# Performance work log

Hardware: AMD Instinct MI355X
Metric: run time of the kernel (lower is better)

The kernel has to match this reference:

```python
import jax, jax.numpy as jnp
import numpy as np

DT = 0.01  # ODE integration step (init kwarg dt)
B, S, I, H, O = 64, 4096, 128, 256, 128


def setup_inputs() -> dict:
    key = jax.random.key(0)
    k0, k1, k2, k3 = jax.random.split(key, 4)
    x = jax.random.normal(k0, (B, S, I), jnp.float32)
    # LTC cell parameters: Linear(in+hidden -> hidden), per-neuron tau and A
    W = jax.random.normal(k1, (I + H, H), jnp.float32) / np.sqrt(I + H)
    b = jnp.zeros((H,), jnp.float32)
    tau = jnp.ones((H,), jnp.float32)
    A = jax.random.normal(k2, (H,), jnp.float32)
    # output Linear(hidden -> out)
    Wo = jax.random.normal(k3, (H, O), jnp.float32) / np.sqrt(H)
    bo = jnp.zeros((O,), jnp.float32)
    return {"x": x, "W": W, "b": b, "tau": tau, "A": A, "Wo": Wo, "bo": bo}


def reference(x, W, b, tau, A, Wo, bo):
    # x: [B, S, I]; recurrence over S with LTC fused semi-implicit ODE step.
    h0 = jnp.zeros((x.shape[0], W.shape[1]), x.dtype)

    def step(h, x_t):
        # f = tanh(Linear([x_t, h]))
        f = jnp.tanh(jnp.concatenate([x_t, h], axis=-1) @ W + b)  # [B, H]
        # fused LTC solver: h' = (h + dt*f*A) / (1 + dt*(1/tau + f))
        h_new = (h + DT * f * A) / (1.0 + DT * (1.0 / tau + f))
        return h_new, None

    h_final, _ = jax.lax.scan(step, h0, jnp.swapaxes(x, 0, 1))  # scan over time
    return h_final @ Wo + bo  # [B, O]
```

## Files before the change

### kernel.cpp

```cpp
#include <hip/hip_runtime.h>
#include <math.h>

#define DT    0.01f
#define B_    64
#define S_    4096
#define I_    128
#define H_    256
#define O_    128

typedef _Float16 f16x8 __attribute__((ext_vector_type(8)));
typedef float    f32x4 __attribute__((ext_vector_type(4)));

#define RPB 64

__global__ __launch_bounds__(256, 2) void xproj_kernel(
    const float* __restrict__ x, const float* __restrict__ W,
    const float* __restrict__ bias, float* __restrict__ xp)
{
  __shared__ __align__(16) float xs[RPB][I_];
  const int j = threadIdx.x;

  float w[I_];
#pragma unroll
  for (int k = 0; k < I_; ++k) w[k] = W[k * H_ + j];
  const float bj = bias[j];

  const size_t row0 = (size_t)blockIdx.x * RPB;

  const float4* src4 = (const float4*)(x + row0 * I_);
  float4* xs4 = (float4*)&xs[0][0];
#pragma unroll
  for (int i = 0; i < (RPB * I_ / 4) / 256; ++i)
    xs4[j + i * 256] = src4[j + i * 256];
  __syncthreads();

  for (int r = 0; r < RPB; r += 4) {
    float a0 = bj, a1 = bj, a2 = bj, a3 = bj;
    const float4* r0 = (const float4*)xs[r + 0];
    const float4* r1 = (const float4*)xs[r + 1];
    const float4* r2 = (const float4*)xs[r + 2];
    const float4* r3 = (const float4*)xs[r + 3];
#pragma unroll
    for (int k4 = 0; k4 < I_ / 4; ++k4) {
      float4 v0 = r0[k4], v1 = r1[k4], v2 = r2[k4], v3 = r3[k4];
      a0 = fmaf(v0.x, w[4*k4+0], a0); a0 = fmaf(v0.y, w[4*k4+1], a0);
      a0 = fmaf(v0.z, w[4*k4+2], a0); a0 = fmaf(v0.w, w[4*k4+3], a0);
      a1 = fmaf(v1.x, w[4*k4+0], a1); a1 = fmaf(v1.y, w[4*k4+1], a1);
      a1 = fmaf(v1.z, w[4*k4+2], a1); a1 = fmaf(v1.w, w[4*k4+3], a1);
      a2 = fmaf(v2.x, w[4*k4+0], a2); a2 = fmaf(v2.y, w[4*k4+1], a2);
      a2 = fmaf(v2.z, w[4*k4+2], a2); a2 = fmaf(v2.w, w[4*k4+3], a2);
      a3 = fmaf(v3.x, w[4*k4+0], a3); a3 = fmaf(v3.y, w[4*k4+1], a3);
      a3 = fmaf(v3.z, w[4*k4+2], a3); a3 = fmaf(v3.w, w[4*k4+3], a3);
    }
    xp[(row0 + r + 0) * H_ + j] = a0;
    xp[(row0 + r + 1) * H_ + j] = a1;
    xp[(row0 + r + 2) * H_ + j] = a2;
    xp[(row0 + r + 3) * H_ + j] = a3;
  }
}

__global__ __launch_bounds__(1024, 4) void ltc_main(
    const float* __restrict__ xp, const float* __restrict__ W,
    const float* __restrict__ tau, const float* __restrict__ A,
    const float* __restrict__ Wo, const float* __restrict__ bo,
    float* __restrict__ out)
{
  const int b  = blockIdx.x;
  const int t  = threadIdx.x;
  const int wv = t >> 6;
  const int l  = t & 63;
  const int g  = l >> 4;
  const int c  = l & 15;
  const int o  = wv * 16 + c;

  f16x8 bw[8];
#pragma unroll
  for (int kt = 0; kt < 8; ++kt)
#pragma unroll
    for (int j = 0; j < 8; ++j)
      bw[kt][j] = (_Float16)W[(I_ + kt * 32 + g * 8 + j) * H_ + o];

  __shared__ __align__(16) _Float16 hs[2][H_];
  __shared__ float hfin[H_];

  const float dtA  = DT * A[o];
  const float base = 1.0f + DT * (1.0f / tau[o]);
  const float rc   = base + DT;
  const float sc   = base - DT;

  const float* xprow = xp + (size_t)b * S_ * H_ + o;

  float h = 0.0f, p = dtA, q = -dtA;
  float xpre = xprow[0];
  if (t < H_) hs[0][t] = (_Float16)0.0f;
  __syncthreads();

#define LTC_BODY(RB, WB, STEP)                                               \
  {                                                                          \
    const _Float16* hb = &hs[RB][g * 8];                                     \
    const int snext = ((STEP) + 1 < S_) ? (STEP) + 1 : (STEP);               \
    const float xnext = xprow[(size_t)snext * H_];                           \
    f16x8 a0_ = *(const f16x8*)(hb);                                         \
    f16x8 a1_ = *(const f16x8*)(hb + 32);                                    \
    f16x8 a2_ = *(const f16x8*)(hb + 64);                                    \
    f16x8 a3_ = *(const f16x8*)(hb + 96);                                    \
    f16x8 a4_ = *(const f16x8*)(hb + 128);                                   \
    f16x8 a5_ = *(const f16x8*)(hb + 160);                                   \
    f16x8 a6_ = *(const f16x8*)(hb + 192);                                   \
    f16x8 a7_ = *(const f16x8*)(hb + 224);                                   \
    f32x4 ac0 = {xpre, xpre, xpre, xpre};                                    \
    f32x4 ac1 = {0.f, 0.f, 0.f, 0.f};                                        \
    __builtin_amdgcn_s_setprio(1);                                           \
    ac0 = __builtin_amdgcn_mfma_f32_16x16x32_f16(a0_, bw[0], ac0, 0, 0, 0);  \
    ac1 = __builtin_amdgcn_mfma_f32_16x16x32_f16(a4_, bw[4], ac1, 0, 0, 0);  \
    ac0 = __builtin_amdgcn_mfma_f32_16x16x32_f16(a1_, bw[1], ac0, 0, 0, 0);  \
    ac1 = __builtin_amdgcn_mfma_f32_16x16x32_f16(a5_, bw[5], ac1, 0, 0, 0);  \
    ac0 = __builtin_amdgcn_mfma_f32_16x16x32_f16(a2_, bw[2], ac0, 0, 0, 0);  \
    ac1 = __builtin_amdgcn_mfma_f32_16x16x32_f16(a6_, bw[6], ac1, 0, 0, 0);  \
    ac0 = __builtin_amdgcn_mfma_f32_16x16x32_f16(a3_, bw[3], ac0, 0, 0, 0);  \
    ac1 = __builtin_amdgcn_mfma_f32_16x16x32_f16(a7_, bw[7], ac1, 0, 0, 0);  \
    __builtin_amdgcn_s_setprio(0);                                           \
    float z = ac0[0] + ac1[0];                                               \
    z = fminf(15.0f, fmaxf(-15.0f, z));                                      \
    const float E = __expf(2.0f * z);                                        \
    const float den = fmaf(E, rc, sc);                                       \
    const float num = fmaf(E, p, q);                                         \
    h = num * __builtin_amdgcn_rcpf(den);                                    \
    p = h + dtA;                                                             \
    q = h - dtA;                                                             \
    if (l < 16) hs[WB][o] = (_Float16)h;                                     \
    xpre = xnext;                                                            \
    __syncthreads();                                                         \
  }

  for (int st = 0; st < S_; st += 2) {
    LTC_BODY(0, 1, st)
    LTC_BODY(1, 0, st + 1)
  }
#undef LTC_BODY

  if (l < 16) hfin[o] = h;
  __syncthreads();

  if (t < O_) {
    float accO = bo[t];
#pragma unroll 8
    for (int hh = 0; hh < H_; ++hh)
      accO = fmaf(hfin[hh], Wo[hh * O_ + t], accO);
    out[b * O_ + t] = accO;
  }
}

__global__ __launch_bounds__(1024) void ltc_inline(
    const float* __restrict__ x, const float* __restrict__ W,
    const float* __restrict__ bias, const float* __restrict__ tau,
    const float* __restrict__ A, const float* __restrict__ Wo,
    const float* __restrict__ bo, float* __restrict__ out)
{
  const int b = blockIdx.x;
  const int t = threadIdx.x;
  const int j = t & (H_ - 1);
  const int c = t >> 8;

  float wh[64], wx[32];
#pragma unroll
  for (int kk = 0; kk < 64; ++kk)
    wh[kk] = W[(I_ + c * 64 + kk) * H_ + j];
#pragma unroll
  for (int kk = 0; kk < 32; ++kk)
    wx[kk] = W[(c * 32 + kk) * H_ + j];

  __shared__ __align__(16) float hsf[H_];
  __shared__ __align__(16) float xsf[I_];
  __shared__ float ps[3][H_];

  float Aj = 0.f, itau = 0.f, bj = 0.f;
  if (c == 0) {
    Aj = A[j];
    itau = 1.0f / tau[j];
    bj = bias[j];
    hsf[j] = 0.0f;
  }
  const float4* xrow4 = (const float4*)(x + (size_t)b * S_ * I_);
  if (t < 32) ((float4*)xsf)[t] = xrow4[t];
  __syncthreads();

  for (int step = 0; step < S_; ++step) {
    float4 xnext4 = make_float4(0.f, 0.f, 0.f, 0.f);
    if (t < 32) {
      const int snext = (step + 1 < S_) ? step + 1 : step;
      xnext4 = xrow4[snext * 32 + t];
    }

    float acc = 0.0f;
#pragma unroll
    for (int kk = 0; kk < 64; kk += 4) {
      float4 h4 = *(const float4*)&hsf[c * 64 + kk];
      acc = fmaf(h4.x, wh[kk + 0], acc);
      acc = fmaf(h4.y, wh[kk + 1], acc);
      acc = fmaf(h4.z, wh[kk + 2], acc);
      acc = fmaf(h4.w, wh[kk + 3], acc);
    }
#pragma unroll
    for (int kk = 0; kk < 32; kk += 4) {
      float4 x4 = *(const float4*)&xsf[c * 32 + kk];
      acc = fmaf(x4.x, wx[kk + 0], acc);
      acc = fmaf(x4.y, wx[kk + 1], acc);
      acc = fmaf(x4.z, wx[kk + 2], acc);
      acc = fmaf(x4.w, wx[kk + 3], acc);
    }

    if (c) ps[c - 1][j] = acc;
    __syncthreads();

    if (t < 32) ((float4*)xsf)[t] = xnext4;
    if (c == 0) {
      const float z = acc + ps[0][j] + ps[1][j] + ps[2][j] + bj;
      const float f = tanhf(z);
      const float hj = hsf[j];
      hsf[j] = (hj + DT * f * Aj) / (1.0f + DT * (itau + f));
    }
    __syncthreads();
  }

  if (t < O_) {
    float acc = bo[t];
#pragma unroll 8
    for (int h = 0; h < H_; ++h)
      acc = fmaf(hsf[h], Wo[h * O_ + t], acc);
    out[b * O_ + t] = acc;
  }
}

extern "C" void kernel_launch(void* const* d_in, const int* in_sizes, int n_in,
                              void* d_out, int out_size, void* d_ws, size_t ws_size,
                              hipStream_t stream) {
  const float* x   = (const float*)d_in[0];
  const float* W   = (const float*)d_in[1];
  const float* b   = (const float*)d_in[2];
  const float* tau = (const float*)d_in[3];
  const float* A   = (const float*)d_in[4];
  const float* Wo  = (const float*)d_in[5];
  const float* bo  = (const float*)d_in[6];
  float* out = (float*)d_out;

  const size_t XP_BYTES = (size_t)B_ * S_ * H_ * sizeof(float);

  if (ws_size >= XP_BYTES) {
    float* xp = (float*)d_ws;
    hipLaunchKernelGGL(xproj_kernel, dim3((B_ * S_) / RPB), dim3(256), 0, stream,
                       x, W, b, xp);
    hipLaunchKernelGGL(ltc_main, dim3(B_), dim3(1024), 0, stream,
                       xp, W, tau, A, Wo, bo, out);
  } else {
    hipLaunchKernelGGL(ltc_inline, dim3(B_), dim3(1024), 0, stream,
                       x, W, b, tau, A, Wo, bo, out);
  }
}
```

Baseline: 1.860 ms.

## Halve recurrent block size and split h·W between MFMA and packed fdot2

The recurrent kernel now runs 512 threads (8 waves) per batch row instead of 1024, so each wave covers 32 output neurons. The first 128 hidden inputs go through MFMA with two accumulators sharing the A operand. The last 128 go through per-lane packed fp16 dot products (fdot2), split across lane pairs and combined with a ds_swizzle. The aim is to cut per-step barrier cost and wave count on the sequential critical path. In exchange each lane does more VALU work and holds more weight registers per step.

Result: slower. 2.247 ms (+20.8%).

```diff
diff --git a/kernel.cpp b/kernel.cpp
--- a/kernel.cpp
+++ b/kernel.cpp
@@ -8,8 +8,23 @@
 #define H_    256
 #define O_    128
 
-typedef _Float16 f16x8 __attribute__((ext_vector_type(8)));
-typedef float    f32x4 __attribute__((ext_vector_type(4)));
+typedef _Float16 f16x8  __attribute__((ext_vector_type(8)));
+typedef _Float16 half2v __attribute__((ext_vector_type(2)));
+typedef float    f32x4  __attribute__((ext_vector_type(4)));
+
+#if defined(__has_builtin)
+#if __has_builtin(__builtin_amdgcn_fdot2)
+#define FDOT2(a, b, c) __builtin_amdgcn_fdot2((a), (b), (c), false)
+#endif
+#endif
+#ifndef FDOT2
+#define FDOT2(a, b, c) \
+  fmaf((float)(a).x, (float)(b).x, fmaf((float)(a).y, (float)(b).y, (c)))
+#endif
+
+static __device__ __forceinline__ half2v mkh2(_Float16 a, _Float16 b) {
+  half2v r; r.x = a; r.y = b; return r;
+}
 
 #define RPB 64
 
@@ -59,7 +74,7 @@
   }
 }
 
-__global__ __launch_bounds__(1024, 4) void ltc_main(
+__global__ __launch_bounds__(512, 2) void ltc_main(
     const float* __restrict__ xp, const float* __restrict__ W,
     const float* __restrict__ tau, const float* __restrict__ A,
     const float* __restrict__ Wo, const float* __restrict__ bo,
@@ -70,15 +85,28 @@
   const int wv = t >> 6;
   const int l  = t & 63;
   const int g  = l >> 4;
+  const int gg = g & 1;
   const int c  = l & 15;
-  const int o  = wv * 16 + c;
-
-  f16x8 bw[8];
-#pragma unroll
-  for (int kt = 0; kt < 8; ++kt)
-#pragma unroll
-    for (int j = 0; j < 8; ++j)
-      bw[kt][j] = (_Float16)W[(I_ + kt * 32 + g * 8 + j) * H_ + o];
+  const int s  = l >> 5;
+  const int o  = wv * 32 + s * 16 + c;
+
+  f16x8 bw[2][4];
+#pragma unroll
+  for (int sg = 0; sg < 2; ++sg)
+#pragma unroll
+    for (int kt = 0; kt < 4; ++kt)
+#pragma unroll
+      for (int j = 0; j < 8; ++j)
+        bw[sg][kt][j] =
+            (_Float16)W[(I_ + kt * 32 + g * 8 + j) * H_ + (wv * 32 + sg * 16 + c)];
+
+  half2v wdd[32];
+#pragma unroll
+  for (int i = 0; i < 32; ++i) {
+    const int k = I_ + 128 + gg * 64 + 2 * i;
+    wdd[i].x = (_Float16)W[k * H_ + o];
+    wdd[i].y = (_Float16)W[(k + 1) * H_ + o];
+  }
 
   __shared__ __align__(16) _Float16 hs[2][H_];
   __shared__ float hfin[H_];
@@ -94,6 +122,12 @@
   float xpre = xprow[0];
   if (t < H_) hs[0][t] = (_Float16)0.0f;
   __syncthreads();
+
+#define DOT8(HV, W0, W1, W2, W3)                                             \
+  dv0 = FDOT2(mkh2(HV[0], HV[1]), W0, dv0);                                  \
+  dv1 = FDOT2(mkh2(HV[2], HV[3]), W1, dv1);                                  \
+  dv0 = FDOT2(mkh2(HV[4], HV[5]), W2, dv0);                                  \
+  dv1 = FDOT2(mkh2(HV[6], HV[7]), W3, dv1);
 
 #define LTC_BODY(RB, WB, STEP)                                               \
   {                                                                          \
@@ -104,23 +138,32 @@
     f16x8 a1_ = *(const f16x8*)(hb + 32);                                    \
     f16x8 a2_ = *(const f16x8*)(hb + 64);                                    \
     f16x8 a3_ = *(const f16x8*)(hb + 96);                                    \
-    f16x8 a4_ = *(const f16x8*)(hb + 128);                                   \
-    f16x8 a5_ = *(const f16x8*)(hb + 160);                                   \
-    f16x8 a6_ = *(const f16x8*)(hb + 192);                                   \
-    f16x8 a7_ = *(const f16x8*)(hb + 224);                                   \
+    const f16x8* h2p = (const f16x8*)&hs[RB][128 + gg * 64];                 \
+    f16x8 hv0 = h2p[0], hv1 = h2p[1], hv2 = h2p[2], hv3 = h2p[3];            \
+    f16x8 hv4 = h2p[4], hv5 = h2p[5], hv6 = h2p[6], hv7 = h2p[7];            \
     f32x4 ac0 = {xpre, xpre, xpre, xpre};                                    \
-    f32x4 ac1 = {0.f, 0.f, 0.f, 0.f};                                        \
-    __builtin_amdgcn_s_setprio(1);                                           \
-    ac0 = __builtin_amdgcn_mfma_f32_16x16x32_f16(a0_, bw[0], ac0, 0, 0, 0);  \
-    ac1 = __builtin_amdgcn_mfma_f32_16x16x32_f16(a4_, bw[4], ac1, 0, 0, 0);  \
-    ac0 = __builtin_amdgcn_mfma_f32_16x16x32_f16(a1_, bw[1], ac0, 0, 0, 0);  \
-    ac1 = __builtin_amdgcn_mfma_f32_16x16x32_f16(a5_, bw[5], ac1, 0, 0, 0);  \
-    ac0 = __builtin_amdgcn_mfma_f32_16x16x32_f16(a2_, bw[2], ac0, 0, 0, 0);  \
-    ac1 = __builtin_amdgcn_mfma_f32_16x16x32_f16(a6_, bw[6], ac1, 0, 0, 0);  \
-    ac0 = __builtin_amdgcn_mfma_f32_16x16x32_f16(a3_, bw[3], ac0, 0, 0, 0);  \
-    ac1 = __builtin_amdgcn_mfma_f32_16x16x32_f16(a7_, bw[7], ac1, 0, 0, 0);  \
-    __builtin_amdgcn_s_setprio(0);                                           \
-    float z = ac0[0] + ac1[0];                                               \
+    f32x4 ac1 = {xpre, xpre, xpre, xpre};                                    \
+    ac0 = __builtin_amdgcn_mfma_f32_16x16x32_f16(a0_, bw[0][0], ac0, 0,0,0); \
+    ac1 = __builtin_amdgcn_mfma_f32_16x16x32_f16(a0_, bw[1][0], ac1, 0,0,0); \
+    ac0 = __builtin_amdgcn_mfma_f32_16x16x32_f16(a1_, bw[0][1], ac0, 0,0,0); \
+    ac1 = __builtin_amdgcn_mfma_f32_16x16x32_f16(a1_, bw[1][1], ac1, 0,0,0); \
+    ac0 = __builtin_amdgcn_mfma_f32_16x16x32_f16(a2_, bw[0][2], ac0, 0,0,0); \
+    ac1 = __builtin_amdgcn_mfma_f32_16x16x32_f16(a2_, bw[1][2], ac1, 0,0,0); \
+    ac0 = __builtin_amdgcn_mfma_f32_16x16x32_f16(a3_, bw[0][3], ac0, 0,0,0); \
+    ac1 = __builtin_amdgcn_mfma_f32_16x16x32_f16(a3_, bw[1][3], ac1, 0,0,0); \
+    float dv0 = 0.f, dv1 = 0.f;                                              \
+    DOT8(hv0, wdd[0],  wdd[1],  wdd[2],  wdd[3])                             \
+    DOT8(hv1, wdd[4],  wdd[5],  wdd[6],  wdd[7])                             \
+    DOT8(hv2, wdd[8],  wdd[9],  wdd[10], wdd[11])                            \
+    DOT8(hv3, wdd[12], wdd[13], wdd[14], wdd[15])                            \
+    DOT8(hv4, wdd[16], wdd[17], wdd[18], wdd[19])                            \
+    DOT8(hv5, wdd[20], wdd[21], wdd[22], wdd[23])                            \
+    DOT8(hv6, wdd[24], wdd[25], wdd[26], wdd[27])                            \
+    DOT8(hv7, wdd[28], wdd[29], wdd[30], wdd[31])                            \
+    float zv = dv0 + dv1;                                                    \
+    zv += __int_as_float(                                                    \
+        __builtin_amdgcn_ds_swizzle(__float_as_int(zv), 0x401F));            \
+    float z = ((l & 32) ? ac1[0] : ac0[0]) + zv;                             \
     z = fminf(15.0f, fmaxf(-15.0f, z));                                      \
     const float E = __expf(2.0f * z);                                        \
     const float den = fmaf(E, rc, sc);                                       \
@@ -128,7 +171,7 @@
     h = num * __builtin_amdgcn_rcpf(den);                                    \
     p = h + dtA;                                                             \
     q = h - dtA;                                                             \
-    if (l < 16) hs[WB][o] = (_Float16)h;                                     \
+    if (!(l & 16)) hs[WB][o] = (_Float16)h;                                  \
     xpre = xnext;                                                            \
     __syncthreads();                                                         \
   }
@@ -138,8 +181,9 @@
     LTC_BODY(1, 0, st + 1)
   }
 #undef LTC_BODY
-
-  if (l < 16) hfin[o] = h;
+#undef DOT8
+
+  if (!(l & 16)) hfin[o] = h;
   __syncthreads();
 
   if (t < O_) {
@@ -250,7 +294,7 @@
     float* xp = (float*)d_ws;
     hipLaunchKernelGGL(xproj_kernel, dim3((B_ * S_) / RPB), dim3(256), 0, stream,
                        x, W, b, xp);
-    hipLaunchKernelGGL(ltc_main, dim3(B_), dim3(1024), 0, stream,
+    hipLaunchKernelGGL(ltc_main, dim3(B_), dim3(512), 0, stream,
                        xp, W, tau, A, Wo, bo, out);
   } else {
     hipLaunchKernelGGL(ltc_inline, dim3(B_), dim3(1024), 0, stream,
```
